# Optimization experiments

Measured on AMD Instinct MI355X. Metric: run time of the kernel, lower is better.

## Reference

```python
import jax, jax.numpy as jnp
import numpy as np

BETA = 0.25
N_CODEBOOK = 2  # hard-coded in the original module
EPS = 1e-12     # torch F.normalize default eps


def l2norm(t):
    # matches torch.nn.functional.normalize(t, p=2, dim=-1)
    n = jnp.linalg.norm(t, axis=-1, keepdims=True)
    return t / jnp.maximum(n, EPS)


def setup_inputs() -> dict:
    key = jax.random.key(0)
    k1, k2 = jax.random.split(key)
    b, n, e_dim, n_e = 16, 256, 1024, 4096
    c = e_dim // N_CODEBOOK
    z = jax.random.normal(k1, (b, n, e_dim), dtype=jnp.float32)
    emb_weight = jax.random.normal(k2, (N_CODEBOOK * n_e, c), dtype=jnp.float32)
    return {"z": z, "emb_weight": emb_weight}


def reference(z, emb_weight):
    b, n, e_dim = z.shape
    f = N_CODEBOOK
    c = e_dim // f
    n_e = emb_weight.shape[0] // f

    # 'b n (f c) -> b f n c'
    zf = jnp.transpose(z.reshape(b, n, f, c), (0, 2, 1, 3))
    # '(b f) c -> b f c' with b=2 (codebooks), f=n_e
    protos = emb_weight.reshape(f, n_e, c)

    zn = l2norm(zf)            # (b, f, n, c)
    pn = l2norm(protos)        # (f, m, c)

    # cosine distance; batch repeat of prototypes is a pure broadcast
    d = 2.0 - 2.0 * jnp.einsum('bfnc,fmc->bfnm', zn, pn)  # (b, f, n, m)
    encoding_indices = jnp.argmin(d, axis=-1)              # (b, f, n) in [0, n_e)

    # faithful to source: indices gather from the FULL (2*n_e) table, no offset
    z_q = l2norm(emb_weight[encoding_indices])             # (b, f, n, c)

    sg = jax.lax.stop_gradient
    loss = BETA * jnp.mean((sg(z_q) - zn) ** 2) + jnp.mean((z_q - sg(zn)) ** 2)

    z_q_st = zn + sg(z_q - zn)                             # straight-through
    # 'b f n c -> b n (f c)'
    z_q_out = jnp.transpose(z_q_st, (0, 2, 1, 3)).reshape(b, n, e_dim)
    return z_q_out, loss, encoding_indices
```

## Files before the change

kernel.cpp:

```cpp
#include <hip/hip_runtime.h>
#include <hip/hip_bf16.h>
#include <stdint.h>

#define FCB 2
#define BB 16
#define NN 256
#define EDIM 1024
#define CC 512
#define NE 4096
#define TOKENS (BB*FCB*NN)
#define ROWS (FCB*NE)
#define OUT_LOSS (BB*NN*EDIM)
#define OUT_IDX  (OUT_LOSS + 1)
#define MARGIN 0.15f

typedef __attribute__((ext_vector_type(8))) short bf16x8;
typedef __attribute__((ext_vector_type(4))) float f32x4;

__device__ __forceinline__ unsigned int ford(float v) {
    unsigned int u = __float_as_uint(v);
    return (u & 0x80000000u) ? ~u : (u | 0x80000000u);
}
__device__ __forceinline__ float unford(unsigned int u) {
    unsigned int b = (u & 0x80000000u) ? (u & 0x7fffffffu) : ~u;
    return __uint_as_float(b);
}


__global__ __launch_bounds__(256) void pack_hi(
    const float* __restrict__ z, const float* __restrict__ emb,
    short* __restrict__ z_hi, short* __restrict__ e_hi,
    float* __restrict__ norm_sq)
{
    int bid = blockIdx.x;
    int tid = threadIdx.x;
    if (bid < 512) {
        __shared__ short lds[8][1032];
        int row0 = bid * 8;
        #pragma unroll
        for (int it = 0; it < 8; ++it) {
            int flat = it * 256 + tid;
            int row = flat >> 8;
            int col4 = flat & 255;
            float4 v = *(const float4*)(z + ((size_t)(row0 + row)) * EDIM + col4 * 4);
            short s0, s1, s2, s3;
            { __hip_bfloat16 h = __float2bfloat16(v.x); s0 = *(short*)&h; }
            { __hip_bfloat16 h = __float2bfloat16(v.y); s1 = *(short*)&h; }
            { __hip_bfloat16 h = __float2bfloat16(v.z); s2 = *(short*)&h; }
            { __hip_bfloat16 h = __float2bfloat16(v.w); s3 = *(short*)&h; }
            short* d = &lds[row][col4 * 4];
            d[0] = s0; d[1] = s1; d[2] = s2; d[3] = s3;
        }
        __syncthreads();
        int R = bid >> 1, mb = (bid & 1) * 8;
        #pragma unroll
        for (int f = 0; f < 2; ++f) {
            #pragma unroll
            for (int it = 0; it < 2; ++it) {
                int unit = it * 256 + tid;
                int ml = unit & 7;
                int Q  = unit >> 3;
                bf16x8 h8 = *(const bf16x8*)&lds[ml][f * 512 + Q * 8];
                size_t u = ((size_t)((f * 256 + R) * 64 + Q)) * 16 + mb + ml;
                *(bf16x8*)(z_hi + u * 8) = h8;
            }
        }
    } else {
        __shared__ float red[256];
        int e = bid - 512;
        int f = e >> 8, R = e & 255;
        int m = tid & 15;
        float ss = 0.f;
        #pragma unroll
        for (int i = 0; i < 4; ++i) {
            int ul = tid + 256 * i;
            int Q = (ul >> 4) & 63;
            const float* s = emb + ((size_t)(f * NE + R * 16 + m)) * CC + Q * 8;
            float4 v0 = *(const float4*)s;
            float4 v1 = *(const float4*)(s + 4);
            float vv[8] = {v0.x, v0.y, v0.z, v0.w, v1.x, v1.y, v1.z, v1.w};
            bf16x8 h8;
            #pragma unroll
            for (int j = 0; j < 8; ++j) {
                __hip_bfloat16 hb = __float2bfloat16(vv[j]);
                h8[j] = *(short*)&hb;
                ss = fmaf(vv[j], vv[j], ss);
            }
            int u = ((f * 256 + R) * 64 + Q) * 16 + m;
            *(bf16x8*)(e_hi + (size_t)u * 8) = h8;
        }
        red[tid] = ss;
        __syncthreads();
        if (tid < 16) {
            float t = 0.f;
            #pragma unroll
            for (int q = 0; q < 16; ++q) t += red[tid + 16 * q];
            norm_sq[f * NE + R * 16 + tid] = t;
        }
    }
}

__global__ __launch_bounds__(256, 3) void gemm_sel(
    const short* __restrict__ zh, const short* __restrict__ eh,
    const float* __restrict__ norm_sq, unsigned int* __restrict__ cand)
{
    __shared__ char smem[32768];
    const int f  = blockIdx.z;
    const int t0 = blockIdx.y * 128;
    const int m0 = blockIdx.x * 128;
    const int tid  = threadIdx.x;
    const int wave = tid >> 6, lane = tid & 63;
    const int wm = wave & 1, wn = wave >> 1;

    f32x4 acc[4][4] = {};

    const short* gptr[8];
    #pragma unroll
    for (int i = 0; i < 8; ++i) {
        int c = wave * 8 + i;
        const short* gsrc = (c < 16) ? zh : eh;
        int cl = c & 15;
        int Rl = cl >> 1, h = cl & 1;
        int R = ((c < 16) ? (t0 >> 4) : (m0 >> 4)) + Rl;
        gptr[i] = gsrc + (((size_t)f * 256 + R) * 64 + h * 4) * 128 + (size_t)lane * 8;
    }

    for (int step = 0; step < 8; ++step) {
        __syncthreads();
        #pragma unroll
        for (int i = 0; i < 8; ++i) {
            __builtin_amdgcn_global_load_lds(
                (const __attribute__((address_space(1))) void*)gptr[i],
                (__attribute__((address_space(3))) void*)(smem + (wave * 8 + i) * 1024),
                16, 0, 0);
            gptr[i] += 1024;
        }
        __syncthreads();

        #pragma unroll
        for (int h = 0; h < 2; ++h) {
            bf16x8 ah[4], bh[4];
            #pragma unroll
            for (int i = 0; i < 4; ++i) {
                ah[i] = *(const bf16x8*)(smem + ((wm*4 + i)*2 + h) * 1024 + lane * 16);
                bh[i] = *(const bf16x8*)(smem + 16384 + ((wn*4 + i)*2 + h) * 1024 + lane * 16);
            }
            #pragma unroll
            for (int i = 0; i < 4; ++i)
                #pragma unroll
                for (int j2 = 0; j2 < 4; ++j2)
                    acc[i][j2] = __builtin_amdgcn_mfma_f32_16x16x32_bf16(ah[i], bh[j2], acc[i][j2], 0, 0, 0);
        }
    }

    float inm[4]; unsigned ccode[4];
    #pragma unroll
    for (int j2 = 0; j2 < 4; ++j2) {
        int col = j2 * 16 + (lane & 15);
        ccode[j2] = (unsigned)(col ^ 63);
        inm[j2] = rsqrtf(norm_sq[f * NE + m0 + wn * 64 + col]);
    }

    #pragma unroll
    for (int i = 0; i < 4; ++i) {
        #pragma unroll
        for (int r = 0; r < 4; ++r) {
            unsigned p1 = 0u, p2 = 0u;
            #pragma unroll
            for (int j2 = 0; j2 < 4; ++j2) {
                float w = acc[i][j2][r] * inm[j2];
                unsigned pw = (ford(w) & 0xFFFFFFC0u) | ccode[j2];
                if (pw > p1) { p2 = p1; p1 = pw; }
                else if (pw > p2) p2 = pw;
            }
            #pragma unroll
            for (int off = 8; off; off >>= 1) {
                unsigned q1 = __shfl_down(p1, off, 16);
                unsigned q2 = __shfl_down(p2, off, 16);
                if (q1 > p1) { unsigned t = p1; p1 = q1; p2 = (t > q2) ? t : q2; }
                else         { p2 = (p2 > q1) ? p2 : q1; }
            }
            if ((lane & 15) == 0) {
                int u = t0 + wm * 64 + i * 16 + (lane >> 4) * 4 + r;
                int b = u >> 8, n = u & 255;
                int gt = ((b * FCB + f) << 8) + n;
                int s = (blockIdx.x << 1) | wn;
                uint2 val; val.x = p1; val.y = p2;
                *(uint2*)(cand + ((size_t)gt << 7) + (s << 1)) = val;
            }
        }
    }
}

__global__ __launch_bounds__(256) void rescore_epilogue(
    const float* __restrict__ z, const float* __restrict__ emb,
    const unsigned int* __restrict__ cand, const float* __restrict__ norm_sq,
    float* __restrict__ out, float* __restrict__ loss_tok)
{
    int t = blockIdx.x * 4 + (threadIdx.x >> 6);
    int lane = threadIdx.x & 63;
    int n = t & 255;
    int f = (t >> 8) & 1;
    int b = t >> 9;
    const float* zrow = z + ((size_t)(b*NN + n))*EDIM + f*CC;
    float4 za = *(const float4*)(zrow + lane * 8);
    float4 zb = *(const float4*)(zrow + lane * 8 + 4);

    uint2 cc = *(const uint2*)(cand + ((size_t)t << 7) + (lane << 1));
    unsigned c1 = cc.x, c2 = cc.y;

    unsigned m1 = (c1 > c2) ? c1 : c2;
    #pragma unroll
    for (int off = 32; off; off >>= 1) {
        unsigned o = __shfl_xor(m1, off);
        if (o > m1) m1 = o;
    }
    float thr = unford(m1) - MARGIN;

    unsigned long long bestp = 0ull;
    #pragma unroll
    for (int rnd = 0; rnd < 2; ++rnd) {
        unsigned u = rnd ? c2 : c1;
        float v = unford(u);
        unsigned long long mask = __ballot(v > thr);
        while (mask) {
            int src = __ffsll((long long)mask) - 1;
            mask &= mask - 1;
            unsigned cu = __shfl(u, src);
            int idx = (src << 6) | ((int)(cu & 63u) ^ 63);
            const float* er = emb + ((size_t)(f * NE + idx)) * CC;
            float4 ea = *(const float4*)(er + lane * 8);
            float4 eb = *(const float4*)(er + lane * 8 + 4);
            float d  = za.x*ea.x + za.y*ea.y + za.z*ea.z + za.w*ea.w
                     + zb.x*eb.x + zb.y*eb.y + zb.z*eb.z + zb.w*eb.w;
            #pragma unroll
            for (int off = 32; off; off >>= 1) d += __shfl_xor(d, off);
            float se = norm_sq[f * NE + idx];
            float vex = d / fmaxf(sqrtf(se), 1e-12f);
            unsigned long long pex = ((unsigned long long)ford(vex) << 32)
                                   | (unsigned int)(~(unsigned int)idx);
            if (pex > bestp) bestp = pex;
        }
    }
    int idxb = (int)(~(unsigned int)bestp);

    const float* er0 = emb + (size_t)idxb * CC;
    float4 ea = *(const float4*)(er0 + lane * 8);
    float4 eb = *(const float4*)(er0 + lane * 8 + 4);
    float inm0 = 1.0f / fmaxf(sqrtf(norm_sq[idxb]), 1e-12f);
    float* orow = out + ((size_t)(b*NN + n))*EDIM + f*CC;
    ea.x *= inm0; ea.y *= inm0; ea.z *= inm0; ea.w *= inm0;
    eb.x *= inm0; eb.y *= inm0; eb.z *= inm0; eb.w *= inm0;
    *(float4*)(orow + lane * 8) = ea;
    *(float4*)(orow + lane * 8 + 4) = eb;
    float s1 = za.x*za.x + za.y*za.y + za.z*za.z + za.w*za.w
             + zb.x*zb.x + zb.y*zb.y + zb.z*zb.z + zb.w*zb.w;
    float s2 = za.x*ea.x + za.y*ea.y + za.z*ea.z + za.w*ea.w
             + zb.x*eb.x + zb.y*eb.y + zb.z*eb.z + zb.w*eb.w;
    #pragma unroll
    for (int off = 32; off; off >>= 1) {
        s1 += __shfl_xor(s1, off);
        s2 += __shfl_xor(s2, off);
    }
    if (lane == 0) {
        float cosv = s2 / fmaxf(sqrtf(s1), 1e-12f);
        loss_tok[t] = 2.0f - 2.0f * cosv;
        out[OUT_IDX + t] = (float)idxb;
    }
}

__global__ __launch_bounds__(256) void loss_reduce(
    const float* __restrict__ loss_tok, float* __restrict__ out)
{
    int tid = threadIdx.x;
    float s = 0.f;
    #pragma unroll
    for (int h = 0; h < 32; ++h) s += loss_tok[h * 256 + tid];
    #pragma unroll
    for (int off = 32; off; off >>= 1) s += __shfl_down(s, off);
    __shared__ float part[4];
    if ((tid & 63) == 0) part[tid >> 6] = s;
    __syncthreads();
    if (tid == 0) {
        float t = part[0] + part[1] + part[2] + part[3];
        out[OUT_LOSS] = t * (1.25f / (float)OUT_LOSS);
    }
}

extern "C" void kernel_launch(void* const* d_in, const int* in_sizes, int n_in,
                              void* d_out, int out_size, void* d_ws, size_t ws_size,
                              hipStream_t stream) {
    const float* z   = (const float*)d_in[0];
    const float* emb = (const float*)d_in[1];
    float* out = (float*)d_out;

    char* ws = (char*)d_ws;
    float* norm_sq = (float*)ws;
    unsigned int* cand = (unsigned int*)(ws + 32768);
    float* loss_tok = (float*)(ws + 32768 + (size_t)4*1024*1024);
    short* z_hi = (short*)(ws + 65536 + (size_t)4*1024*1024);
    short* e_hi = z_hi + (size_t)FCB * NE * CC;

    pack_hi<<<1024, 256, 0, stream>>>(z, emb, z_hi, e_hi, norm_sq);
    gemm_sel<<<dim3(NE/128, NE/128, FCB), 256, 0, stream>>>(z_hi, e_hi, norm_sq, cand);
    rescore_epilogue<<<TOKENS/4, 256, 0, stream>>>(z, emb, cand, norm_sq, out, loss_tok);
    loss_reduce<<<1, 256, 0, stream>>>(loss_tok, out);
}
```

Baseline: 145.4 us.

## Fuse loss reduction into rescore via last-block counter, widen pack blocks

Removes the separate single-block loss_reduce launch by having the last-finishing rescore block, found through an atomic counter that pack_hi resets, sum the per-token losses. pack_hi moves to 512 threads per block with half the loop iterations. In gemm_sel, global pointers are now recomputed each step instead of being kept in an array of eight, which lowers register pressure but adds address arithmetic. The fused reduction adds atomics and fences to every rescore block.

```diff
diff --git a/kernel.cpp b/kernel.cpp
--- a/kernel.cpp
+++ b/kernel.cpp
@@ -27,19 +27,20 @@
 }
 
 
-__global__ __launch_bounds__(256) void pack_hi(
+__global__ __launch_bounds__(512) void pack_hi(
     const float* __restrict__ z, const float* __restrict__ emb,
     short* __restrict__ z_hi, short* __restrict__ e_hi,
-    float* __restrict__ norm_sq)
+    float* __restrict__ norm_sq, unsigned int* __restrict__ counter)
 {
     int bid = blockIdx.x;
     int tid = threadIdx.x;
+    if (bid == 0 && tid == 0) *counter = 0u;
     if (bid < 512) {
         __shared__ short lds[8][1032];
         int row0 = bid * 8;
         #pragma unroll
-        for (int it = 0; it < 8; ++it) {
-            int flat = it * 256 + tid;
+        for (int it = 0; it < 4; ++it) {
+            int flat = it * 512 + tid;
             int row = flat >> 8;
             int col4 = flat & 255;
             float4 v = *(const float4*)(z + ((size_t)(row0 + row)) * EDIM + col4 * 4);
@@ -53,27 +54,23 @@
         }
         __syncthreads();
         int R = bid >> 1, mb = (bid & 1) * 8;
+        int ml = tid & 7;
+        int Q  = tid >> 3;
         #pragma unroll
         for (int f = 0; f < 2; ++f) {
-            #pragma unroll
-            for (int it = 0; it < 2; ++it) {
-                int unit = it * 256 + tid;
-                int ml = unit & 7;
-                int Q  = unit >> 3;
-                bf16x8 h8 = *(const bf16x8*)&lds[ml][f * 512 + Q * 8];
-                size_t u = ((size_t)((f * 256 + R) * 64 + Q)) * 16 + mb + ml;
-                *(bf16x8*)(z_hi + u * 8) = h8;
-            }
+            bf16x8 h8 = *(const bf16x8*)&lds[ml][f * 512 + Q * 8];
+            size_t u = ((size_t)((f * 256 + R) * 64 + Q)) * 16 + mb + ml;
+            *(bf16x8*)(z_hi + u * 8) = h8;
         }
     } else {
-        __shared__ float red[256];
+        __shared__ float red[512];
         int e = bid - 512;
         int f = e >> 8, R = e & 255;
         int m = tid & 15;
         float ss = 0.f;
         #pragma unroll
-        for (int i = 0; i < 4; ++i) {
-            int ul = tid + 256 * i;
+        for (int i = 0; i < 2; ++i) {
+            int ul = tid + 512 * i;
             int Q = (ul >> 4) & 63;
             const float* s = emb + ((size_t)(f * NE + R * 16 + m)) * CC + Q * 8;
             float4 v0 = *(const float4*)s;
@@ -94,7 +91,7 @@
         if (tid < 16) {
             float t = 0.f;
             #pragma unroll
-            for (int q = 0; q < 16; ++q) t += red[tid + 16 * q];
+            for (int q = 0; q < 32; ++q) t += red[tid + 16 * q];
             norm_sq[f * NE + R * 16 + tid] = t;
         }
     }
@@ -114,26 +111,22 @@
 
     f32x4 acc[4][4] = {};
 
-    const short* gptr[8];
-    #pragma unroll
-    for (int i = 0; i < 8; ++i) {
-        int c = wave * 8 + i;
-        const short* gsrc = (c < 16) ? zh : eh;
-        int cl = c & 15;
-        int Rl = cl >> 1, h = cl & 1;
-        int R = ((c < 16) ? (t0 >> 4) : (m0 >> 4)) + Rl;
-        gptr[i] = gsrc + (((size_t)f * 256 + R) * 64 + h * 4) * 128 + (size_t)lane * 8;
-    }
-
     for (int step = 0; step < 8; ++step) {
         __syncthreads();
         #pragma unroll
         for (int i = 0; i < 8; ++i) {
+            int c = wave * 8 + i;
+            const short* gsrc = (c < 16) ? zh : eh;
+            int cl = c & 15;
+            int Rl = cl >> 1, h = cl & 1;
+            int R = ((c < 16) ? (t0 >> 4) : (m0 >> 4)) + Rl;
+            int qb = step * 8 + h * 4;
+            const short* g = gsrc
+                + (((size_t)f * 256 + R) * 64 + qb) * 128 + (size_t)lane * 8;
             __builtin_amdgcn_global_load_lds(
-                (const __attribute__((address_space(1))) void*)gptr[i],
-                (__attribute__((address_space(3))) void*)(smem + (wave * 8 + i) * 1024),
+                (const __attribute__((address_space(1))) void*)g,
+                (__attribute__((address_space(3))) void*)(smem + c * 1024),
                 16, 0, 0);
-            gptr[i] += 1024;
         }
         __syncthreads();
 
@@ -195,7 +188,8 @@
 __global__ __launch_bounds__(256) void rescore_epilogue(
     const float* __restrict__ z, const float* __restrict__ emb,
     const unsigned int* __restrict__ cand, const float* __restrict__ norm_sq,
-    float* __restrict__ out, float* __restrict__ loss_tok)
+    float* __restrict__ out, float* __restrict__ loss_tok,
+    unsigned int* __restrict__ counter)
 {
     int t = blockIdx.x * 4 + (threadIdx.x >> 6);
     int lane = threadIdx.x & 63;
@@ -264,26 +258,35 @@
     }
     if (lane == 0) {
         float cosv = s2 / fmaxf(sqrtf(s1), 1e-12f);
-        loss_tok[t] = 2.0f - 2.0f * cosv;
+        __hip_atomic_store(&loss_tok[t], 2.0f - 2.0f * cosv,
+                           __ATOMIC_RELAXED, __HIP_MEMORY_SCOPE_AGENT);
         out[OUT_IDX + t] = (float)idxb;
     }
-}
-
-__global__ __launch_bounds__(256) void loss_reduce(
-    const float* __restrict__ loss_tok, float* __restrict__ out)
-{
-    int tid = threadIdx.x;
-    float s = 0.f;
-    #pragma unroll
-    for (int h = 0; h < 32; ++h) s += loss_tok[h * 256 + tid];
-    #pragma unroll
-    for (int off = 32; off; off >>= 1) s += __shfl_down(s, off);
+
+    __shared__ int lastf;
     __shared__ float part[4];
-    if ((tid & 63) == 0) part[tid >> 6] = s;
     __syncthreads();
-    if (tid == 0) {
-        float t = part[0] + part[1] + part[2] + part[3];
-        out[OUT_LOSS] = t * (1.25f / (float)OUT_LOSS);
+    if (threadIdx.x == 0) {
+        __threadfence();
+        lastf = (atomicAdd(counter, 1u) == (unsigned)(gridDim.x - 1));
+    }
+    __syncthreads();
+    if (lastf) {
+        __threadfence();
+        int tid = threadIdx.x;
+        float s = 0.f;
+        #pragma unroll
+        for (int h = 0; h < 32; ++h)
+            s += __hip_atomic_load(&loss_tok[h * 256 + tid],
+                                   __ATOMIC_RELAXED, __HIP_MEMORY_SCOPE_AGENT);
+        #pragma unroll
+        for (int off = 32; off; off >>= 1) s += __shfl_down(s, off);
+        if ((tid & 63) == 0) part[tid >> 6] = s;
+        __syncthreads();
+        if (tid == 0) {
+            float tt = part[0] + part[1] + part[2] + part[3];
+            out[OUT_LOSS] = tt * (1.25f / (float)OUT_LOSS);
+        }
     }
 }
 
@@ -298,11 +301,11 @@
     float* norm_sq = (float*)ws;
     unsigned int* cand = (unsigned int*)(ws + 32768);
     float* loss_tok = (float*)(ws + 32768 + (size_t)4*1024*1024);
-    short* z_hi = (short*)(ws + 65536 + (size_t)4*1024*1024);
+    unsigned int* counter = (unsigned int*)(ws + 65536 + (size_t)4*1024*1024);
+    short* z_hi = (short*)(ws + 69632 + (size_t)4*1024*1024);
     short* e_hi = z_hi + (size_t)FCB * NE * CC;
 
-    pack_hi<<<1024, 256, 0, stream>>>(z, emb, z_hi, e_hi, norm_sq);
+    pack_hi<<<1024, 512, 0, stream>>>(z, emb, z_hi, e_hi, norm_sq, counter);
     gemm_sel<<<dim3(NE/128, NE/128, FCB), 256, 0, stream>>>(z_hi, e_hi, norm_sq, cand);
-    rescore_epilogue<<<TOKENS/4, 256, 0, stream>>>(z, emb, cand, norm_sq, out, loss_tok);
-    loss_reduce<<<1, 256, 0, stream>>>(loss_tok, out);
-}
+    rescore_epilogue<<<TOKENS/4, 256, 0, stream>>>(z, emb, cand, norm_sq, out, loss_tok, counter);
+}
```

New measurement: 217.0 us. 49.3% more time.
